# Optimization experiments

Hardware: AMD Instinct MI355X
Metric: run time of the kernel (lower is better)

Reference implementation:

```python
import jax, jax.numpy as jnp
import numpy as np

N = 50000
E = 800000
C = 64


def setup_inputs() -> dict:
    key = jax.random.key(0)
    ks = jax.random.split(key, 16)
    s = 0.05
    x = jax.random.normal(ks[0], (N, C), jnp.float32)
    edge_attr = jax.random.uniform(ks[1], (E, 4), dtype=jnp.float32)
    edge_index = jax.random.randint(ks[2], (2, E), 0, N)
    deg_hist = jax.random.uniform(ks[3], (N,), dtype=jnp.float32) * 32.0
    W = jax.random.normal(ks[4], (C, C), jnp.float32) * s          # self.weight[0]
    We = jax.random.normal(ks[5], (3, C), jnp.float32) * s         # edge_encoder
    be = jnp.zeros((C,), jnp.float32)
    Wpre = jax.random.normal(ks[6], (3 * C, C), jnp.float32) * s   # pre_nn Linear
    bpre = jnp.zeros((C,), jnp.float32)
    A_S = 4 * 3  # aggregators * scalers
    Wpost = jax.random.normal(ks[7], ((A_S + 1) * C, C), jnp.float32) * s
    bpost = jnp.zeros((C,), jnp.float32)
    Wih = jax.random.normal(ks[8], (C, 3 * C), jnp.float32) * s    # GRUCell input weights (transposed)
    bih = jnp.zeros((3 * C,), jnp.float32)
    Whh = jax.random.normal(ks[9], (C, 3 * C), jnp.float32) * s    # GRUCell hidden weights (transposed)
    bhh = jnp.zeros((3 * C,), jnp.float32)
    return dict(x=x, edge_attr=edge_attr, deg_hist=deg_hist, W=W, We=We, be=be,
                Wpre=Wpre, bpre=bpre, Wpost=Wpost, bpost=bpost,
                Wih=Wih, bih=bih, Whh=Whh, bhh=bhh, edge_index=edge_index)


def reference(x, edge_attr, deg_hist, W, We, be, Wpre, bpre, Wpost, bpost,
              Wih, bih, Whh, bhh, edge_index):
    n_nodes = x.shape[0]
    # gated path: m = x @ weight[0]
    m = x @ W  # [N, C]
    src, dst = edge_index[0], edge_index[1]
    # message: edge-weight scaling + edge encoder + pre-MLP (single Linear)
    ew = edge_attr[:, 3:4]                         # [E, 1]
    ea = edge_attr[:, :3] @ We + be                # [E, C]
    xi = ew * m[dst]                               # x_i (target)
    xj = ew * m[src]                               # x_j (source)
    ea = ew * ea
    h = jnp.concatenate([xi, xj, ea], axis=-1) @ Wpre + bpre  # [E, C]
    # multi-aggregator scatter: mean, min, max, std (keyed by target node)
    ones = jnp.ones((h.shape[0],), h.dtype)
    cnt = jax.ops.segment_sum(ones, dst, num_segments=n_nodes)       # [N]
    safe = jnp.maximum(cnt, 1.0)[:, None]
    s1 = jax.ops.segment_sum(h, dst, num_segments=n_nodes)
    s2 = jax.ops.segment_sum(h * h, dst, num_segments=n_nodes)
    mean = s1 / safe
    mean_sq = s2 / safe
    std = jnp.sqrt(jax.nn.relu(mean_sq - mean * mean) + 1e-5)
    has = (cnt > 0)[:, None]
    mn = jnp.where(has, jax.ops.segment_min(h, dst, num_segments=n_nodes), 0.0)
    mx = jnp.where(has, jax.ops.segment_max(h, dst, num_segments=n_nodes), 0.0)
    agg = jnp.concatenate([mean, mn, mx, std], axis=-1)  # [N, 4C]
    # degree scalers (faithfully replicating the cumulative reassignment in the torch loop)
    deg = jnp.maximum(cnt, 1.0)[:, None]
    avg_log = jnp.mean(jnp.log(deg_hist + 1.0))
    logd = jnp.log(deg + 1.0)
    o1 = agg                          # identity
    o2 = o1 * (logd / avg_log)        # amplification
    o3 = o2 * (avg_log / logd)        # attenuation applied on top of o2 (torch bug, kept)
    out = jnp.concatenate([o1, o2, o3], axis=-1)          # [N, 12C]
    # post-MLP on cat([m, aggregated])
    out = jnp.concatenate([m, out], axis=-1) @ Wpost + bpost  # [N, C]
    # GRUCell(out, x): torch gate order r, z, n
    gi = out @ Wih + bih
    gh = x @ Whh + bhh
    ir, iz, i_n = jnp.split(gi, 3, axis=-1)
    hr, hz, h_n = jnp.split(gh, 3, axis=-1)
    r = jax.nn.sigmoid(ir + hr)
    z = jax.nn.sigmoid(iz + hz)
    n = jnp.tanh(i_n + r * h_n)
    return (1.0 - z) * n + z * x
```

## Files before the change

### kernel.cpp

```cpp
#include <hip/hip_runtime.h>
#include <math.h>

#define NN  50000
#define NNP 50048
#define NE  800000

#define B_BG1   0u
#define B_BG2A  49152u
#define B_BG2B  90112u
#define B_BG3   122880u
#define B_WE2   147456u
#define B_BE2   148224u
#define B_B3    148480u
#define B_SUML  149248u
#define B_XB    149504u
#define B_NF    6555648u
#define B_GH    19367936u
#define B_A2    38586368u
#define B_S2F   70617088u
#define B_CNT   70817280u
#define B_OFFS  71017280u
#define B_RANK  71217408u
#define B_EL2   74417408u
#define B_PART  80817408u

#define SCAN_B  196

typedef __attribute__((ext_vector_type(8))) short s8v;
typedef __attribute__((ext_vector_type(4))) short s4v;
typedef __attribute__((ext_vector_type(4))) float f4v;

__device__ inline short f2b(float f){
    union { float f; unsigned u; } v; v.f = f;
    unsigned r = v.u + 0x7fffu + ((v.u >> 16) & 1u);
    return (short)(r >> 16);
}
__device__ inline float b2f(short b){
    union { unsigned u; float f; } v; v.u = ((unsigned)(unsigned short)b) << 16;
    return v.f;
}

__global__ __launch_bounds__(256) void k_prep(const float* __restrict__ x,
    const float* __restrict__ dh, const int* __restrict__ dstA,
    const float* __restrict__ W, const float* __restrict__ Wpre,
    const float* __restrict__ We, const float* __restrict__ be,
    const float* __restrict__ bpost, const float* __restrict__ Wpost,
    const float* __restrict__ Wih, const float* __restrict__ bih,
    const float* __restrict__ Whh, int* __restrict__ cnt,
    int* __restrict__ rank, unsigned char* __restrict__ wsb)
{
    __shared__ float sred[4];
    int b = blockIdx.x, t = threadIdx.x;
    {
        int e = b * 256 + t;
        rank[e] = atomicAdd(&cnt[dstA[e]], 1);
    }

    if (b < 38) {
        int idx = b * 256 + t;
        if (idx < 3072) {
            short* dst = (short*)(wsb + B_BG1);
            int lane = idx & 63, ts = idx >> 6;
            int tt = ts >> 1, s = ts & 1;
            int quad = lane >> 4, l15 = lane & 15, n = tt*16 + l15;
            for (int j = 0; j < 8; ++j) {
                int k = s*32 + quad*8 + j;
                float v;
                if (n < 64)       v = W[k*64 + n];
                else if (n < 128) { v = 0.f; for (int c = 0; c < 64; ++c) v += W[k*64+c]*Wpre[c*64 + (n-64)]; }
                else if (n < 192) { v = 0.f; for (int c = 0; c < 64; ++c) v += W[k*64+c]*Wpre[4096 + c*64 + (n-128)]; }
                else              v = Whh[k*192 + (n-192)];
                dst[((size_t)ts*64 + lane)*8 + j] = f2b(v);
            }
        } else if (idx < 5632) {
            int id = idx - 3072;
            short* dst = (short*)(wsb + B_BG2A);
            int lane = id & 63, ts = id >> 6;
            int quad = lane >> 4, l15 = lane & 15;
            int tt = ts / 10, s = ts % 10;
            int n = tt*16 + l15;
            for (int j = 0; j < 8; ++j) {
                int k = s*32 + quad*8 + j;
                float v;
                if (k < 64) v = Wpost[k*64 + n];
                else {
                    int kk = k - 64, ch = kk >> 2, st = kk & 3;
                    int ok = 64 + st*64 + ch;
                    v = Wpost[ok*64 + n] + Wpost[(ok + 512)*64 + n];
                }
                dst[((size_t)ts*64 + lane)*8 + j] = f2b(v);
            }
        } else if (idx < 7680) {
            int id = idx - 5632;
            short* dst = (short*)(wsb + B_BG2B);
            int lane = id & 63, ts = id >> 6;
            int quad = lane >> 4, l15 = lane & 15;
            int tt = ts / 8, s = ts % 8;
            int n = tt*16 + l15;
            for (int j = 0; j < 8; ++j) {
                int k = s*32 + quad*8 + j;
                int ch = k >> 2, st = k & 3;
                int ok = 320 + st*64 + ch;
                dst[((size_t)ts*64 + lane)*8 + j] = f2b(Wpost[ok*64 + n]);
            }
        } else if (idx < 9216) {
            int id = idx - 7680;
            short* dst = (short*)(wsb + B_BG3);
            int lane = id & 63, ts = id >> 6;
            int tt = ts >> 1, s = ts & 1;
            int quad = lane >> 4, l15 = lane & 15, n = tt*16 + l15;
            for (int j = 0; j < 8; ++j) {
                int k = s*32 + quad*8 + j;
                dst[((size_t)ts*64 + lane)*8 + j] = f2b(Wih[k*192 + n]);
            }
        } else if (idx < 9408) {
            int t2 = idx - 9216; int kk = t2 >> 6, j = t2 & 63;
            float v = 0.f;
            for (int c = 0; c < 64; ++c) v += We[kk*64 + c] * Wpre[(128+c)*64 + j];
            ((float*)(wsb + B_WE2))[t2] = v;
        } else if (idx < 9472) {
            int j = idx - 9408;
            float v = 0.f;
            for (int c = 0; c < 64; ++c) v += be[c] * Wpre[(128+c)*64 + j];
            ((float*)(wsb + B_BE2))[j] = v;
        } else if (idx < 9664) {
            int j = idx - 9472;
            float v = bih[j];
            for (int k = 0; k < 64; ++k) v += bpost[k] * Wih[k*192 + j];
            ((float*)(wsb + B_B3))[j] = v;
        }
    } else if (b < 1601) {
        int i = (b - 38) * 256 + t;
        if (i < 400000) {
            const float4* xp = (const float4*)(x + (size_t)i * 8);
            float4 p0 = xp[0], p1 = xp[1];
            s8v o;
            o[0]=f2b(p0.x); o[1]=f2b(p0.y); o[2]=f2b(p0.z); o[3]=f2b(p0.w);
            o[4]=f2b(p1.x); o[5]=f2b(p1.y); o[6]=f2b(p1.z); o[7]=f2b(p1.w);
            *(s8v*)((short*)(wsb + B_XB) + (size_t)i * 8) = o;
        }
    } else if (b < 1797) {
        int i = (b - 1601) * 256 + t;
        float v = (i < NN) ? logf(dh[i] + 1.f) : 0.f;
        #pragma unroll
        for (int m = 32; m >= 1; m >>= 1) v += __shfl_xor(v, m, 64);
        if ((t & 63) == 0) sred[t >> 6] = v;
        __syncthreads();
        if (t == 0) atomicAdd((float*)(wsb + B_SUML), sred[0]+sred[1]+sred[2]+sred[3]);
    }
}

__global__ __launch_bounds__(256) void k_scanA(const int* __restrict__ cnt,
    int* __restrict__ offs, int* __restrict__ part)
{
    __shared__ int sh[256];
    int t = threadIdx.x, i = blockIdx.x * 256 + t;
    int v = (i < NN) ? cnt[i] : 0;
    sh[t] = v; __syncthreads();
    #pragma unroll
    for (int o = 1; o < 256; o <<= 1) {
        int u = (t >= o) ? sh[t - o] : 0;
        __syncthreads();
        sh[t] += u;
        __syncthreads();
    }
    if (i < NN) offs[i] = sh[t] - v;
    if (t == 255) part[blockIdx.x] = sh[255];
}

__global__ __launch_bounds__(256) void k_scanC(const int* __restrict__ part,
    int* __restrict__ offs)
{
    __shared__ int sh[256];
    int b = blockIdx.x, t = threadIdx.x;
    int v = (t < SCAN_B) ? part[t] : 0;
    sh[t] = v; __syncthreads();
    #pragma unroll
    for (int o = 1; o < 256; o <<= 1) {
        int u = (t >= o) ? sh[t - o] : 0;
        __syncthreads();
        sh[t] += u;
        __syncthreads();
    }
    int base = (b == 0) ? 0 : sh[b - 1];
    int i = b * 256 + t;
    if (i < NN) offs[i] += base;
    if (b == 0 && t == 0) offs[NN] = NE;
}

__global__ __launch_bounds__(256) void k_scatter(const int* __restrict__ srcA,
    const int* __restrict__ dstA, const int* __restrict__ rank,
    const int* __restrict__ offs, int2* __restrict__ el2)
{
    int e = blockIdx.x * 256 + threadIdx.x;
    int dst = dstA[e];
    int r   = rank[e];
    int src = srcA[e];
    el2[offs[dst] + r] = make_int2(e, src);
}

__global__ __launch_bounds__(256) void k_g1(unsigned char* __restrict__ wsb)
{
    const short* xb = (const short*)(wsb + B_XB);
    const short* bf = (const short*)(wsb + B_BG1);
    short* a2 = (short*)(wsb + B_A2);
    short* nf = (short*)(wsb + B_NF);
    short* gh = (short*)(wsb + B_GH);
    int w = threadIdx.x >> 6, lane = threadIdx.x & 63;
    int quad = lane >> 4, l15 = lane & 15;
    int R0 = blockIdx.x * 64 + w * 16;
    const short* arow = xb + (size_t)(R0 + l15) * 64 + quad * 8;
    s8v a0 = *(const s8v*)(arow);
    s8v a1 = *(const s8v*)(arow + 32);
    f4v acc[24];
    #pragma unroll
    for (int t = 0; t < 24; ++t) acc[t] = (f4v){0.f,0.f,0.f,0.f};
    #pragma unroll
    for (int t = 0; t < 24; ++t) {
        s8v b0 = *(const s8v*)(bf + ((size_t)(t*2+0)*64 + lane)*8);
        s8v b1 = *(const s8v*)(bf + ((size_t)(t*2+1)*64 + lane)*8);
        acc[t] = __builtin_amdgcn_mfma_f32_16x16x32_bf16(a0, b0, acc[t], 0, 0, 0);
        acc[t] = __builtin_amdgcn_mfma_f32_16x16x32_bf16(a1, b1, acc[t], 0, 0, 0);
    }
    #pragma unroll
    for (int t = 0; t < 24; ++t) {
        #pragma unroll
        for (int r = 0; r < 4; ++r) {
            int row = R0 + quad*4 + r;
            if (row >= NN) continue;
            short v = f2b(acc[t][r]);
            if (t < 4)       a2[(size_t)row*320 + t*16 + l15] = v;
            else if (t < 12) nf[(size_t)row*128 + (t-4)*16 + l15] = v;
            else             gh[(size_t)row*192 + (t-12)*16 + l15] = v;
        }
    }
}

__global__ __launch_bounds__(256) void k_agg(const float* __restrict__ eattr,
    const float* __restrict__ bpre, unsigned char* __restrict__ wsb)
{
    __shared__ float4 sEA[4][64];
    __shared__ int    sOFF[4][64];
    int lane = threadIdx.x & 63;
    int w    = threadIdx.x >> 6;
    int wid  = blockIdx.x * 4 + w;
    const int* offs = (const int*)(wsb + B_OFFS);
    const int2* el2 = (const int2*)(wsb + B_EL2);
    const unsigned char* nfb = wsb + B_NF;
    const short* nf = (const short*)(wsb + B_NF);
    const float* we2p = (const float*)(wsb + B_WE2);
    float we0 = we2p[lane], we1 = we2p[64 + lane], we2v = we2p[128 + lane];
    float be2l = ((const float*)(wsb + B_BE2))[lane];
    float bprel = bpre[lane];
    float rcpavg = (float)NN / ((const float*)(wsb + B_SUML))[0];
    const float4* e4 = (const float4*)eattr;
    unsigned laneoff = 128u + 2u * (unsigned)lane;
    short* a2b = (short*)(wsb + B_A2);
    float* s2f = (float*)(wsb + B_S2F);

    for (int n = wid; n < NN; n += 8192) {
        float md2l = b2f(nf[(size_t)n * 128 + lane]);
        float tbase = md2l + be2l;
        int o0 = offs[n], o1e = offs[n + 1];
        float s = 0.f, ss = 0.f, mn = INFINITY, mx = -INFINITY;
        for (int base = o0; base < o1e; base += 64) {
            int cnt = o1e - base; if (cnt > 64) cnt = 64;
            if (lane < cnt) {
                int2 es = el2[base + lane];
                sOFF[w][lane] = es.y << 8;
                sEA[w][lane]  = e4[es.x];
            }
            for (int d0 = 0; d0 < cnt; d0 += 8) {
                float msv[8];
                #pragma unroll
                for (int u = 0; u < 8; ++u) {
                    int d = d0 + u; if (d > cnt - 1) d = cnt - 1;
                    unsigned off = (unsigned)sOFF[w][d] + laneoff;
                    msv[u] = b2f(*(const short*)(nfb + off));
                }
                #pragma unroll
                for (int u = 0; u < 8; ++u) {
                    int d = d0 + u;
                    if (d < cnt) {
                        float4 ea = sEA[w][d];
                        float t = tbase + msv[u];
                        t = fmaf(ea.x, we0, t);
                        t = fmaf(ea.y, we1, t);
                        t = fmaf(ea.z, we2v, t);
                        float h = fmaf(ea.w, t, bprel);
                        s += h; ss = fmaf(h, h, ss);
                        mn = fminf(mn, h); mx = fmaxf(mx, h);
                    }
                }
            }
        }
        int deg = o1e - o0;
        float safe = (float)(deg > 0 ? deg : 1);
        float mean = s / safe;
        float var  = ss / safe - mean * mean;
        float stdv = sqrtf(fmaxf(var, 0.f) + 1e-5f);
        if (deg == 0) { mn = 0.f; mx = 0.f; }
        s4v o; o[0] = f2b(mean); o[1] = f2b(mn); o[2] = f2b(mx); o[3] = f2b(stdv);
        *(s4v*)(a2b + (size_t)n * 320 + 64 + (lane << 2)) = o;
        if (lane == 0) s2f[n] = logf(safe + 1.f) * rcpavg;
    }
}

__global__ __launch_bounds__(256) void k_g23(const float* __restrict__ x,
    const float* __restrict__ bhh, unsigned char* __restrict__ wsb,
    float* __restrict__ out)
{
    __shared__ short sm[64 * 72];
    __shared__ float sS2[64];
    const short* a2  = (const short*)(wsb + B_A2);
    const short* bgA = (const short*)(wsb + B_BG2A);
    const short* bgB = (const short*)(wsb + B_BG2B);
    const short* bg3 = (const short*)(wsb + B_BG3);
    const short* gh  = (const short*)(wsb + B_GH);
    const float* b3  = (const float*)(wsb + B_B3);
    const float* s2f = (const float*)(wsb + B_S2F);
    int w = threadIdx.x >> 6, lane = threadIdx.x & 63;
    int quad = lane >> 4, l15 = lane & 15;
    int R0 = blockIdx.x * 64 + w * 16;

    {
        int i = threadIdx.x;
        if (i < 64) {
            int row = blockIdx.x * 64 + i;
            sS2[i] = (row < NN) ? s2f[row] : 0.f;
        }
    }

    const short* aBase = a2 + (size_t)(R0 + l15) * 320 + quad * 8;
    f4v acc1[4], acc2[4];
    #pragma unroll
    for (int t = 0; t < 4; ++t) { acc1[t] = (f4v){0.f,0.f,0.f,0.f}; acc2[t] = (f4v){0.f,0.f,0.f,0.f}; }
    #pragma unroll 2
    for (int s = 0; s < 10; ++s) {
        s8v a = *(const s8v*)(aBase + s * 32);
        #pragma unroll
        for (int t = 0; t < 4; ++t) {
            s8v b = *(const s8v*)(bgA + ((size_t)(t*10 + s)*64 + lane)*8);
            acc1[t] = __builtin_amdgcn_mfma_f32_16x16x32_bf16(a, b, acc1[t], 0, 0, 0);
        }
    }
    #pragma unroll 2
    for (int s = 0; s < 8; ++s) {
        s8v a = *(const s8v*)(aBase + 64 + s * 32);
        #pragma unroll
        for (int t = 0; t < 4; ++t) {
            s8v b = *(const s8v*)(bgB + ((size_t)(t*8 + s)*64 + lane)*8);
            acc2[t] = __builtin_amdgcn_mfma_f32_16x16x32_bf16(a, b, acc2[t], 0, 0, 0);
        }
    }
    __syncthreads();
    #pragma unroll
    for (int t = 0; t < 4; ++t)
        #pragma unroll
        for (int r = 0; r < 4; ++r) {
            int lr = w*16 + quad*4 + r;
            float v = acc1[t][r] + sS2[lr] * acc2[t][r];
            sm[lr * 72 + t*16 + l15] = f2b(v);
        }
    __syncthreads();

    const short* arow = sm + (w*16 + l15) * 72 + quad * 8;
    s8v a0 = *(const s8v*)(arow);
    s8v a1 = *(const s8v*)(arow + 32);
    f4v acc[12];
    #pragma unroll
    for (int t = 0; t < 12; ++t) acc[t] = (f4v){0.f,0.f,0.f,0.f};
    #pragma unroll
    for (int t = 0; t < 12; ++t) {
        s8v b0 = *(const s8v*)(bg3 + ((size_t)(t*2+0)*64 + lane)*8);
        s8v b1 = *(const s8v*)(bg3 + ((size_t)(t*2+1)*64 + lane)*8);
        acc[t] = __builtin_amdgcn_mfma_f32_16x16x32_bf16(a0, b0, acc[t], 0, 0, 0);
        acc[t] = __builtin_amdgcn_mfma_f32_16x16x32_bf16(a1, b1, acc[t], 0, 0, 0);
    }
    #pragma unroll
    for (int t = 0; t < 4; ++t) {
        #pragma unroll
        for (int r = 0; r < 4; ++r) {
            int row = R0 + quad*4 + r;
            if (row >= NN) continue;
            int c = t*16 + l15;
            float ir  = acc[t][r]   + b3[c];
            float iz  = acc[t+4][r] + b3[64 + c];
            float inn = acc[t+8][r] + b3[128 + c];
            const short* g = gh + (size_t)row * 192;
            float hr = b2f(g[c])       + bhh[c];
            float hz = b2f(g[64 + c])  + bhh[64 + c];
            float hn = b2f(g[128 + c]) + bhh[128 + c];
            float rr = 1.f / (1.f + expf(-(ir + hr)));
            float zz = 1.f / (1.f + expf(-(iz + hz)));
            float nn = tanhf(inn + rr * hn);
            out[(size_t)row*64 + c] = (1.f - zz)*nn + zz*x[(size_t)row*64 + c];
        }
    }
}

extern "C" void kernel_launch(void* const* d_in, const int* in_sizes, int n_in,
                              void* d_out, int out_size, void* d_ws, size_t ws_size,
                              hipStream_t stream)
{
    const float* x     = (const float*)d_in[0];
    const float* eattr = (const float*)d_in[1];
    const float* dh    = (const float*)d_in[2];
    const float* W     = (const float*)d_in[3];
    const float* We    = (const float*)d_in[4];
    const float* be    = (const float*)d_in[5];
    const float* Wpre  = (const float*)d_in[6];
    const float* bpre  = (const float*)d_in[7];
    const float* Wpost = (const float*)d_in[8];
    const float* bpost = (const float*)d_in[9];
    const float* Wih   = (const float*)d_in[10];
    const float* bih   = (const float*)d_in[11];
    const float* Whh   = (const float*)d_in[12];
    const float* bhh   = (const float*)d_in[13];
    const int*   eidx  = (const int*)d_in[14];
    unsigned char* wsb = (unsigned char*)d_ws;
    float* out = (float*)d_out;
    const int* srcA = eidx;
    const int* dstA = eidx + NE;
    int* cnt  = (int*)(wsb + B_CNT);
    int* offs = (int*)(wsb + B_OFFS);
    int* rank = (int*)(wsb + B_RANK);
    int2* el2 = (int2*)(wsb + B_EL2);
    int* part = (int*)(wsb + B_PART);

    hipMemsetAsync(wsb + B_SUML, 0, 4, stream);
    hipMemsetAsync(cnt, 0, NN * sizeof(int), stream);

    k_prep    <<<3125, 256, 0, stream>>>(x, dh, dstA, W, Wpre, We, be, bpost,
                                         Wpost, Wih, bih, Whh, cnt, rank, wsb);
    k_scanA   <<<SCAN_B, 256, 0, stream>>>(cnt, offs, part);
    k_scanC   <<<SCAN_B, 256, 0, stream>>>(part, offs);
    k_scatter <<<NE/256, 256, 0, stream>>>(srcA, dstA, rank, offs, el2);
    k_g1      <<<NNP/64, 256, 0, stream>>>(wsb);
    k_agg     <<<2048, 256, 0, stream>>>(eattr, bpre, wsb);
    k_g23     <<<NNP/64, 256, 0, stream>>>(x, bhh, wsb, out);
}
```

Measured before the change: 256.5 us.

## Replicate per-node degree counters to reduce atomic contention in CSR build

```diff
diff --git a/kernel.cpp b/kernel.cpp
--- a/kernel.cpp
+++ b/kernel.cpp
@@ -4,6 +4,7 @@
 #define NN  50000
 #define NNP 50048
 #define NE  800000
+#define REP 16
 
 #define B_BG1   0u
 #define B_BG2A  49152u
@@ -19,10 +20,11 @@
 #define B_A2    38586368u
 #define B_S2F   70617088u
 #define B_CNT   70817280u
-#define B_OFFS  71017280u
-#define B_RANK  71217408u
-#define B_EL2   74417408u
-#define B_PART  80817408u
+#define B_OFFS  74017280u
+#define B_RANK  74217344u
+#define B_ROFF  77417344u
+#define B_EL2   80617344u
+#define B_PART  87017344u
 
 #define SCAN_B  196
 
@@ -53,7 +55,8 @@
     int b = blockIdx.x, t = threadIdx.x;
     {
         int e = b * 256 + t;
-        rank[e] = atomicAdd(&cnt[dstA[e]], 1);
+        int r = b & (REP - 1);
+        rank[e] = atomicAdd(&cnt[r * NN + dstA[e]], 1);
     }
 
     if (b < 38) {
@@ -151,11 +154,19 @@
 }
 
 __global__ __launch_bounds__(256) void k_scanA(const int* __restrict__ cnt,
-    int* __restrict__ offs, int* __restrict__ part)
+    int* __restrict__ offs, int* __restrict__ roff, int* __restrict__ part)
 {
     __shared__ int sh[256];
     int t = threadIdx.x, i = blockIdx.x * 256 + t;
-    int v = (i < NN) ? cnt[i] : 0;
+    int v = 0;
+    int pre[REP];
+    if (i < NN) {
+        #pragma unroll
+        for (int r = 0; r < REP; ++r) {
+            pre[r] = v;
+            v += cnt[r * NN + i];
+        }
+    }
     sh[t] = v; __syncthreads();
     #pragma unroll
     for (int o = 1; o < 256; o <<= 1) {
@@ -164,12 +175,18 @@
         sh[t] += u;
         __syncthreads();
     }
-    if (i < NN) offs[i] = sh[t] - v;
+    if (i < NN) {
+        offs[i] = sh[t] - v;
+        int4* rp = (int4*)(roff + (size_t)i * REP);
+        #pragma unroll
+        for (int q = 0; q < REP/4; ++q)
+            rp[q] = make_int4(pre[q*4], pre[q*4+1], pre[q*4+2], pre[q*4+3]);
+    }
     if (t == 255) part[blockIdx.x] = sh[255];
 }
 
 __global__ __launch_bounds__(256) void k_scanC(const int* __restrict__ part,
-    int* __restrict__ offs)
+    int* __restrict__ offs, int* __restrict__ roff)
 {
     __shared__ int sh[256];
     int b = blockIdx.x, t = threadIdx.x;
@@ -184,19 +201,29 @@
     }
     int base = (b == 0) ? 0 : sh[b - 1];
     int i = b * 256 + t;
-    if (i < NN) offs[i] += base;
+    if (i < NN) {
+        int fo = offs[i] + base;
+        offs[i] = fo;
+        int4* rp = (int4*)(roff + (size_t)i * REP);
+        #pragma unroll
+        for (int q = 0; q < REP/4; ++q) {
+            int4 r4 = rp[q];
+            r4.x += fo; r4.y += fo; r4.z += fo; r4.w += fo;
+            rp[q] = r4;
+        }
+    }
     if (b == 0 && t == 0) offs[NN] = NE;
 }
 
 __global__ __launch_bounds__(256) void k_scatter(const int* __restrict__ srcA,
     const int* __restrict__ dstA, const int* __restrict__ rank,
-    const int* __restrict__ offs, int2* __restrict__ el2)
+    const int* __restrict__ roff, int2* __restrict__ el2)
 {
     int e = blockIdx.x * 256 + threadIdx.x;
+    int r = blockIdx.x & (REP - 1);
     int dst = dstA[e];
-    int r   = rank[e];
-    int src = srcA[e];
-    el2[offs[dst] + r] = make_int2(e, src);
+    int p = roff[dst * REP + r] + rank[e];
+    el2[p] = make_int2(e, srcA[e]);
 }
 
 __global__ __launch_bounds__(256) void k_g1(unsigned char* __restrict__ wsb)
@@ -425,17 +452,18 @@
     int* cnt  = (int*)(wsb + B_CNT);
     int* offs = (int*)(wsb + B_OFFS);
     int* rank = (int*)(wsb + B_RANK);
+    int* roff = (int*)(wsb + B_ROFF);
     int2* el2 = (int2*)(wsb + B_EL2);
     int* part = (int*)(wsb + B_PART);
 
     hipMemsetAsync(wsb + B_SUML, 0, 4, stream);
-    hipMemsetAsync(cnt, 0, NN * sizeof(int), stream);
+    hipMemsetAsync(cnt, 0, REP * NN * sizeof(int), stream);
 
     k_prep    <<<3125, 256, 0, stream>>>(x, dh, dstA, W, Wpre, We, be, bpost,
                                          Wpost, Wih, bih, Whh, cnt, rank, wsb);
-    k_scanA   <<<SCAN_B, 256, 0, stream>>>(cnt, offs, part);
-    k_scanC   <<<SCAN_B, 256, 0, stream>>>(part, offs);
-    k_scatter <<<NE/256, 256, 0, stream>>>(srcA, dstA, rank, offs, el2);
+    k_scanA   <<<SCAN_B, 256, 0, stream>>>(cnt, offs, roff, part);
+    k_scanC   <<<SCAN_B, 256, 0, stream>>>(part, offs, roff);
+    k_scatter <<<NE/256, 256, 0, stream>>>(srcA, dstA, rank, roff, el2);
     k_g1      <<<NNP/64, 256, 0, stream>>>(wsb);
     k_agg     <<<2048, 256, 0, stream>>>(eattr, bpre, wsb);
     k_g23     <<<NNP/64, 256, 0, stream>>>(x, bhh, wsb, out);
```

New measurement: 261.6 us. 1.02x slower.
